# Kernel optimization log

Hardware: AMD Instinct MI355X
Metric: run time of the kernel (lower is better)

## Reference

```python
import jax, jax.numpy as jnp
import numpy as np

N_NODES = 50000
N_EDGES = 800000
N_INPUT = 512
N_HIDDEN = 64


def setup_inputs() -> dict:
    key = jax.random.key(0)
    ks = jax.random.split(key, 6)
    x = jax.random.normal(ks[0], (1, N_NODES, N_INPUT), dtype=jnp.float32)
    edge_rows = jax.random.randint(ks[1], (N_EDGES,), 0, N_NODES, dtype=jnp.int64)
    edge_cols = jax.random.randint(ks[2], (N_EDGES,), 0, N_NODES, dtype=jnp.int64)
    edge_vals = jax.random.uniform(ks[3], (N_EDGES,), dtype=jnp.float32)
    # xavier_normal_ on fc.weight: std = sqrt(2 / (fan_in + fan_out))
    std = float(np.sqrt(2.0 / (N_INPUT + N_HIDDEN)))
    W = jax.random.normal(ks[4], (N_HIDDEN, N_INPUT), dtype=jnp.float32) * std
    b = jnp.zeros((N_HIDDEN,), dtype=jnp.float32)
    alpha = jnp.full((1,), 0.25, dtype=jnp.float32)  # PReLU default init
    return {"x": x, "edge_rows": edge_rows, "edge_cols": edge_cols,
            "edge_vals": edge_vals, "W": W, "b": b, "alpha": alpha}


def reference(x, edge_rows, edge_cols, edge_vals, W, b, alpha):
    # Linear projection: [1, N, F_in] @ [F_in, F_out] -> [1, N, F_out]
    h = jnp.einsum('bnf,hf->bnh', x, W) + b
    h = jnp.squeeze(h, 0)  # [N, F_out]
    # spmm(adj, h): out[i] = sum_e vals[e] * h[cols[e]] for rows[e] == i
    msgs = edge_vals[:, None] * h[edge_cols]  # [E, F_out]
    agg = jax.ops.segment_sum(msgs, edge_rows, num_segments=N_NODES)  # [N, F_out]
    out = agg[None, :, :]  # [1, N, F_out]
    # PReLU with shared alpha
    return jnp.where(out >= 0, out, alpha * out)
```

## Files before the change

### kernel.cpp

```cpp
#include <hip/hip_runtime.h>

#define NODES 50000
#define NEDGES 800000
#define NIN 512
#define NHID 64

#define NB 391
#define BCAP 2560
#define EB 4096
#define NBA 196

typedef __attribute__((ext_vector_type(8))) short short8v;
typedef __attribute__((ext_vector_type(8))) unsigned short ushort8v;
typedef __attribute__((ext_vector_type(4))) float f32x4;
typedef __attribute__((ext_vector_type(4))) unsigned int uint4v;

#define H_OFF    0
#define WBF_OFF  1600000
#define GCUR_OFF 1616384
#define RMETA_OFF 1616896
#define ECV2_OFF 1716896

__device__ inline unsigned short f2bf(float f) {
  unsigned u = __builtin_bit_cast(unsigned, f);
  u += 0x7FFF + ((u >> 16) & 1);
  return (unsigned short)(u >> 16);
}
__device__ inline float bf2f(unsigned short u) {
  return __builtin_bit_cast(float, (unsigned)u << 16);
}

__global__ __launch_bounds__(256) void init_kernel(
    const float* __restrict__ W, unsigned int* __restrict__ wbf,
    int* __restrict__ gcur)
{
  int i = blockIdx.x * 256 + threadIdx.x;
  if (i < NIN * NHID / 2) {
    float2 w = reinterpret_cast<const float2*>(W)[i];
    wbf[i] = (unsigned)f2bf(w.x) | ((unsigned)f2bf(w.y) << 16);
  }
  if (i < NB) gcur[i] = 0;
}

__global__ __launch_bounds__(256) void binA_kernel(
    const int* __restrict__ rows, const int* __restrict__ cols,
    const float* __restrict__ vals, int* __restrict__ gcur,
    int2* __restrict__ ecv2)
{
  __shared__ int hist[NB];
  __shared__ unsigned short slots[EB];
  int bid = blockIdx.x;
  int tid = (int)threadIdx.x;
  int e0 = bid * EB;

  for (int i = tid; i < NB; i += 256) hist[i] = 0;
  __syncthreads();
  #pragma unroll 4
  for (int k = 0; k < EB / 256; ++k) {
    int i = e0 + k * 256 + tid;
    if (i < NEDGES) {
      int r = rows[i];
      int s = atomicAdd(&hist[r >> 7], 1);
      slots[k * 256 + tid] = (unsigned short)s;
    }
  }
  __syncthreads();
  for (int i = tid; i < NB; i += 256) {
    int c = hist[i];
    hist[i] = c ? atomicAdd(&gcur[i], c) : 0;
  }
  __syncthreads();
  #pragma unroll 4
  for (int k = 0; k < EB / 256; ++k) {
    int i = e0 + k * 256 + tid;
    if (i < NEDGES) {
      int r = rows[i];
      int bkt = r >> 7;
      int sl = hist[bkt] + (int)slots[k * 256 + tid];
      if (sl < BCAP)
        ecv2[(long)bkt * BCAP + sl] =
            make_int2(cols[i] | ((r & 127) << 17), __float_as_int(vals[i]));
    }
  }
}

__global__ __launch_bounds__(256, 2) void gemm_kernel(
    const float* __restrict__ x, const unsigned short* __restrict__ wbf,
    const float* __restrict__ b, unsigned short* __restrict__ h)
{
  int gw = blockIdx.x * 4 + ((int)threadIdx.x >> 6);
  if (gw >= NODES / 16) return;
  int lane = (int)(threadIdx.x & 63);
  int r16 = lane & 15;
  int kg  = lane >> 4;

  const float4* xp = reinterpret_cast<const float4*>(
      x + (long)(gw * 16 + r16) * NIN + kg * 8);
  const unsigned short* wp = wbf + (long)r16 * NIN + kg * 8;

  float4 xb[32];
  #pragma unroll
  for (int s = 0; s < 16; ++s) {
    xb[2 * s]     = xp[8 * s];
    xb[2 * s + 1] = xp[8 * s + 1];
  }
  {
    float* xf = reinterpret_cast<float*>(xb);
    #pragma unroll
    for (int i = 0; i < 128; ++i) asm volatile("" : "+v"(xf[i]));
  }
  __builtin_amdgcn_sched_barrier(0);

  f32x4 acc[4] = {{0,0,0,0},{0,0,0,0},{0,0,0,0},{0,0,0,0}};

  #pragma unroll
  for (int s = 0; s < 16; ++s) {
    float4 a0 = xb[2 * s];
    float4 a1 = xb[2 * s + 1];
    unsigned p0, p1, p2, p3;
    asm("v_cvt_pk_bf16_f32 %0, %1, %2" : "=v"(p0) : "v"(a0.x), "v"(a0.y));
    asm("v_cvt_pk_bf16_f32 %0, %1, %2" : "=v"(p1) : "v"(a0.z), "v"(a0.w));
    asm("v_cvt_pk_bf16_f32 %0, %1, %2" : "=v"(p2) : "v"(a1.x), "v"(a1.y));
    asm("v_cvt_pk_bf16_f32 %0, %1, %2" : "=v"(p3) : "v"(a1.z), "v"(a1.w));
    uint4v ap = {p0, p1, p2, p3};
    short8v af = __builtin_bit_cast(short8v, ap);
    #pragma unroll
    for (int ft = 0; ft < 4; ++ft) {
      short8v bfr = *reinterpret_cast<const short8v*>(
          wp + (long)ft * 16 * NIN + s * 32);
      acc[ft] = __builtin_amdgcn_mfma_f32_16x16x32_bf16(af, bfr, acc[ft], 0, 0, 0);
    }
  }

  int n0 = gw * 16 + kg * 4;
  #pragma unroll
  for (int ft = 0; ft < 4; ++ft) {
    float bias = b[ft * 16 + r16];
    #pragma unroll
    for (int r = 0; r < 4; ++r)
      h[(long)(n0 + r) * NHID + ft * 16 + r16] = f2bf(acc[ft][r] + bias);
  }
}

__global__ __launch_bounds__(256) void sortb_kernel(
    const int* __restrict__ gcur, int2* __restrict__ ecv2,
    int2* __restrict__ rowmeta)
{
  __shared__ int2 ed[BCAP];
  __shared__ unsigned short slots[BCAP];
  __shared__ int hist[128], base[128], stmp[128];
  int bkt = blockIdx.x;
  int tid = (int)threadIdx.x;

  int n = gcur[bkt];
  if (n > BCAP) n = BCAP;
  int2* bptr = ecv2 + (long)bkt * BCAP;

  if (tid < 128) hist[tid] = 0;
  __syncthreads();

  for (int i = tid; i < n; i += 256) {
    int2 e = bptr[i];
    ed[i] = e;
    int rl = e.x >> 17;
    slots[i] = (unsigned short)atomicAdd(&hist[rl], 1);
  }
  __syncthreads();

  int v = (tid < 128) ? hist[tid] : 0;
  if (tid < 128) stmp[tid] = v;
  __syncthreads();
  for (int d = 1; d < 128; d <<= 1) {
    int t = (tid < 128 && tid >= d) ? stmp[tid - d] : 0;
    __syncthreads();
    if (tid < 128) stmp[tid] += t;
    __syncthreads();
  }
  if (tid < 128) base[tid] = stmp[tid] - v;
  __syncthreads();

  for (int i = tid; i < n; i += 256) {
    int2 e = ed[i];
    int rl = e.x >> 17;
    int pos = base[rl] + (int)slots[i];
    bptr[pos] = make_int2(e.x & 0x1FFFF, e.y);
  }

  if (tid < 128) {
    int row = bkt * 128 + tid;
    if (row < NODES)
      rowmeta[row] = make_int2(bkt * BCAP + base[tid], hist[tid]);
  }
}

__global__ __launch_bounds__(256) void gather_kernel(
    const int2* __restrict__ rowmeta, const int2* __restrict__ ecv2,
    const unsigned short* __restrict__ h, const float* __restrict__ alpha,
    float* __restrict__ out)
{
  int wid = (int)((blockIdx.x * 256 + threadIdx.x) >> 6);
  if (wid >= NODES) return;
  int lane = (int)(threadIdx.x & 63);
  int eg = lane >> 3;
  int fo = lane & 7;
  int2 m = rowmeta[wid];
  int deg = m.y;
  const int2* base = ecv2 + m.x;
  float a = alpha[0];

  float acc[8] = {0.f, 0.f, 0.f, 0.f, 0.f, 0.f, 0.f, 0.f};
  int j = eg;
  int2 e = (j < deg) ? base[j] : make_int2(0, 0);
  while (j < deg) {
    int2 en = (j + 8 < deg) ? base[j + 8] : make_int2(0, 0);
    float v = __int_as_float(e.y);
    ushort8v hv = *reinterpret_cast<const ushort8v*>(&h[(long)e.x * NHID + fo * 8]);
    #pragma unroll
    for (int k = 0; k < 8; ++k)
      acc[k] = fmaf(v, bf2f(hv[k]), acc[k]);
    e = en;
    j += 8;
  }

  #pragma unroll
  for (int k = 0; k < 8; ++k) {
    acc[k] += __shfl_xor(acc[k], 8);
    acc[k] += __shfl_xor(acc[k], 16);
    acc[k] += __shfl_xor(acc[k], 32);
  }

  if (eg == 0) {
    float4 o0, o1;
    o0.x = acc[0] >= 0.f ? acc[0] : a * acc[0];
    o0.y = acc[1] >= 0.f ? acc[1] : a * acc[1];
    o0.z = acc[2] >= 0.f ? acc[2] : a * acc[2];
    o0.w = acc[3] >= 0.f ? acc[3] : a * acc[3];
    o1.x = acc[4] >= 0.f ? acc[4] : a * acc[4];
    o1.y = acc[5] >= 0.f ? acc[5] : a * acc[5];
    o1.z = acc[6] >= 0.f ? acc[6] : a * acc[6];
    o1.w = acc[7] >= 0.f ? acc[7] : a * acc[7];
    *reinterpret_cast<float4*>(&out[(long)wid * NHID + fo * 8]) = o0;
    *reinterpret_cast<float4*>(&out[(long)wid * NHID + fo * 8 + 4]) = o1;
  }
}

extern "C" void kernel_launch(void* const* d_in, const int* in_sizes, int n_in,
                              void* d_out, int out_size, void* d_ws, size_t ws_size,
                              hipStream_t stream) {
  const float* x     = (const float*)d_in[0];
  const int*   rows  = (const int*)d_in[1];
  const int*   cols  = (const int*)d_in[2];
  const float* vals  = (const float*)d_in[3];
  const float* W     = (const float*)d_in[4];
  const float* b     = (const float*)d_in[5];
  const float* alpha = (const float*)d_in[6];
  float* out = (float*)d_out;

  float* wsf = (float*)d_ws;
  unsigned short* h     = (unsigned short*)(wsf + H_OFF);
  unsigned int*   wbf   = (unsigned int*)(wsf + WBF_OFF);
  int*            gcur  = (int*)(wsf + GCUR_OFF);
  int2*           rmeta = (int2*)(wsf + RMETA_OFF);
  int2*           ecv2  = (int2*)(wsf + ECV2_OFF);

  init_kernel<<<64, 256, 0, stream>>>(W, wbf, gcur);
  binA_kernel<<<NBA, 256, 0, stream>>>(rows, cols, vals, gcur, ecv2);
  gemm_kernel<<<(NODES / 16 + 3) / 4, 256, 0, stream>>>(
      x, (const unsigned short*)wbf, b, h);
  sortb_kernel<<<NB, 256, 0, stream>>>(gcur, ecv2, rmeta);
  gather_kernel<<<NODES * 64 / 256, 256, 0, stream>>>(rmeta, ecv2, h, alpha, out);
}
```

Before: 106.1 us.

## Stage x tile through LDS as bf16 with coalesced loads in GEMM

The GEMM kernel now has each 256-thread block load a 64-row tile of x with fully coalesced float4 reads, convert it to bf16 and store it in padded shared memory. MFMA A-fragments are then read from LDS, replacing the strided per-lane register prefetch of 128 floats. The aim is better global-load coalescing and far fewer VGPRs, at the cost of 68KB of LDS per block, a block-wide barrier, and no overlap between loading and compute within a block.

```diff
diff --git a/kernel.cpp b/kernel.cpp
--- a/kernel.cpp
+++ b/kernel.cpp
@@ -9,6 +9,8 @@
 #define BCAP 2560
 #define EB 4096
 #define NBA 196
+
+#define XSTR 268
 
 typedef __attribute__((ext_vector_type(8))) short short8v;
 typedef __attribute__((ext_vector_type(8))) unsigned short ushort8v;
@@ -84,61 +86,61 @@
   }
 }
 
-__global__ __launch_bounds__(256, 2) void gemm_kernel(
+__global__ __launch_bounds__(256) void gemm_kernel(
     const float* __restrict__ x, const unsigned short* __restrict__ wbf,
     const float* __restrict__ b, unsigned short* __restrict__ h)
 {
-  int gw = blockIdx.x * 4 + ((int)threadIdx.x >> 6);
-  if (gw >= NODES / 16) return;
-  int lane = (int)(threadIdx.x & 63);
+  __shared__ unsigned int xls[64 * XSTR];
+  int blk = blockIdx.x;
+  int tid = (int)threadIdx.x;
+
+  #pragma unroll 8
+  for (int c = 0; c < 32; ++c) {
+    int idx = c * 256 + tid;
+    int lrow = idx >> 7;
+    int k4 = idx & 127;
+    long grow = (long)blk * 64 + lrow;
+    if (grow >= NODES) grow = NODES - 1;
+    float4 v = *reinterpret_cast<const float4*>(x + grow * NIN + k4 * 4);
+    unsigned lo, hi;
+    asm("v_cvt_pk_bf16_f32 %0, %1, %2" : "=v"(lo) : "v"(v.x), "v"(v.y));
+    asm("v_cvt_pk_bf16_f32 %0, %1, %2" : "=v"(hi) : "v"(v.z), "v"(v.w));
+    *reinterpret_cast<uint2*>(&xls[lrow * XSTR + k4 * 2]) = make_uint2(lo, hi);
+  }
+  __syncthreads();
+
+  int wv = tid >> 6;
+  int lane = tid & 63;
   int r16 = lane & 15;
   int kg  = lane >> 4;
-
-  const float4* xp = reinterpret_cast<const float4*>(
-      x + (long)(gw * 16 + r16) * NIN + kg * 8);
+  int lrow = wv * 16 + r16;
+  const unsigned int* rowp = &xls[lrow * XSTR];
   const unsigned short* wp = wbf + (long)r16 * NIN + kg * 8;
 
-  float4 xb[32];
+  f32x4 acc[4] = {{0,0,0,0},{0,0,0,0},{0,0,0,0},{0,0,0,0}};
+
   #pragma unroll
-  for (int s = 0; s < 16; ++s) {
-    xb[2 * s]     = xp[8 * s];
-    xb[2 * s + 1] = xp[8 * s + 1];
-  }
-  {
-    float* xf = reinterpret_cast<float*>(xb);
-    #pragma unroll
-    for (int i = 0; i < 128; ++i) asm volatile("" : "+v"(xf[i]));
-  }
-  __builtin_amdgcn_sched_barrier(0);
-
-  f32x4 acc[4] = {{0,0,0,0},{0,0,0,0},{0,0,0,0},{0,0,0,0}};
-
-  #pragma unroll
-  for (int s = 0; s < 16; ++s) {
-    float4 a0 = xb[2 * s];
-    float4 a1 = xb[2 * s + 1];
-    unsigned p0, p1, p2, p3;
-    asm("v_cvt_pk_bf16_f32 %0, %1, %2" : "=v"(p0) : "v"(a0.x), "v"(a0.y));
-    asm("v_cvt_pk_bf16_f32 %0, %1, %2" : "=v"(p1) : "v"(a0.z), "v"(a0.w));
-    asm("v_cvt_pk_bf16_f32 %0, %1, %2" : "=v"(p2) : "v"(a1.x), "v"(a1.y));
-    asm("v_cvt_pk_bf16_f32 %0, %1, %2" : "=v"(p3) : "v"(a1.z), "v"(a1.w));
-    uint4v ap = {p0, p1, p2, p3};
+  for (int m = 0; m < 16; ++m) {
+    uint4v ap = *reinterpret_cast<const uint4v*>(rowp + m * 16 + kg * 4);
     short8v af = __builtin_bit_cast(short8v, ap);
     #pragma unroll
     for (int ft = 0; ft < 4; ++ft) {
       short8v bfr = *reinterpret_cast<const short8v*>(
-          wp + (long)ft * 16 * NIN + s * 32);
+          wp + (long)ft * 16 * NIN + m * 32);
       acc[ft] = __builtin_amdgcn_mfma_f32_16x16x32_bf16(af, bfr, acc[ft], 0, 0, 0);
     }
   }
 
-  int n0 = gw * 16 + kg * 4;
+  int nbase = blk * 64 + wv * 16 + kg * 4;
   #pragma unroll
   for (int ft = 0; ft < 4; ++ft) {
     float bias = b[ft * 16 + r16];
     #pragma unroll
-    for (int r = 0; r < 4; ++r)
-      h[(long)(n0 + r) * NHID + ft * 16 + r16] = f2bf(acc[ft][r] + bias);
+    for (int r = 0; r < 4; ++r) {
+      int node = nbase + r;
+      if (node < NODES)
+        h[(long)node * NHID + ft * 16 + r16] = f2bf(acc[ft][r] + bias);
+    }
   }
 }
 
@@ -265,7 +267,7 @@
 
   init_kernel<<<64, 256, 0, stream>>>(W, wbf, gcur);
   binA_kernel<<<NBA, 256, 0, stream>>>(rows, cols, vals, gcur, ecv2);
-  gemm_kernel<<<(NODES / 16 + 3) / 4, 256, 0, stream>>>(
+  gemm_kernel<<<(NODES + 63) / 64, 256, 0, stream>>>(
       x, (const unsigned short*)wbf, b, h);
   sortb_kernel<<<NB, 256, 0, stream>>>(gcur, ecv2, rmeta);
   gather_kernel<<<NODES * 64 / 256, 256, 0, stream>>>(rmeta, ecv2, h, alpha, out);
```

After: 107.1 us. No clear change (+0.9%).
